# Performance work log

Measured on AMD Instinct MI355X. Metric: run time of the kernel, lower is better.

Reference implementation:

```python
import jax, jax.numpy as jnp
import numpy as np

H = 256          # hidden_dim
E = 300          # embedding_dim
V = 50000        # vocab size
MLP = 1024       # mlp_dim
BS, L, S, AMB = 32, 128, 127, 32
INV_TEMP = 1.0
EPS = 1e-8


def setup_inputs() -> dict:
    key = jax.random.key(0)
    ks = jax.random.split(key, 12)
    inp = {
        "W": jax.random.normal(ks[0], (5 * H, E), jnp.float32) * 0.02,
        "U": jax.random.normal(ks[1], (5 * H, 2 * H), jnp.float32) * 0.02,
        "b": jnp.zeros((5 * H,), jnp.float32),
        "energy_u": jax.random.normal(ks[2], (H,), jnp.float32) * 0.1 + 0.01,
        "word_embeddings": jax.random.normal(ks[3], (V, E), jnp.float32),
        "w1": jax.random.normal(ks[4], (MLP, 2 * H), jnp.float32) * 0.02,
        "b1": jnp.zeros((MLP,), jnp.float32),
        "w2": jax.random.normal(ks[5], (3, MLP), jnp.float32) * 0.02,
        "b2": jnp.zeros((3,), jnp.float32),
        "sentences1": jax.random.randint(ks[6], (BS, L), 0, V, jnp.int32),
        "ops1": jax.random.randint(ks[7], (BS, S, AMB, 2), 0, L, jnp.int32),
        "sentences2": jax.random.randint(ks[8], (BS, L), 0, V, jnp.int32),
        "ops2": jax.random.randint(ks[9], (BS, S, AMB, 2), 0, L, jnp.int32),
    }
    return inp


def _ch(pre, ccL, ccR):
    # pre: [..., 5H]; tree-LSTM cell with two forget gates
    i = jax.nn.sigmoid(pre[..., :H])
    fL = jax.nn.sigmoid(pre[..., H:2 * H])
    fR = jax.nn.sigmoid(pre[..., 2 * H:3 * H])
    o = jax.nn.sigmoid(pre[..., 3 * H:4 * H])
    u = jnp.tanh(pre[..., 4 * H:])
    c = fL * ccL + fR * ccR + i * u
    return c, o * jnp.tanh(c)


def _encode(W, U, b, energy_u, word_embeddings, sentences, ops):
    bs = sentences.shape[0]
    # leaf cells: preact = W @ emb + b, combine with zero children
    emb = word_embeddings[sentences]                      # [bs, L, E]
    pre = jnp.einsum('ble,fe->blf', emb, W) + b           # [bs, L, 5H]
    c0, h0 = _ch(pre, 0.0, 0.0)
    chart = jnp.zeros((bs, L + S, 2 * H), jnp.float32)
    chart = chart.at[:, :L, :H].set(c0).at[:, :L, H:].set(h0)

    bidx = jnp.arange(bs)[:, None, None]                  # [bs,1,1]
    u_norm = jnp.linalg.norm(energy_u)

    def step(chart, inp):
        step_idx, op = inp                                # op: [bs, amb, 2]
        entries = chart[bidx, op]                         # [bs, amb, 2, 2H]
        ccL = entries[:, :, 0, :H]
        ccR = entries[:, :, 1, :H]
        hh = entries[..., H:].reshape(bs, AMB, 2 * H)     # concat(hL, hR)
        pre = jnp.einsum('bah,fh->baf', hh, U) + b        # [bs, amb, 5H]
        c, h = _ch(pre, ccL, ccR)
        # cosine similarity against energy_u (torch eps=1e-8)
        num = jnp.einsum('bah,h->ba', h, energy_u)
        den = jnp.maximum(jnp.linalg.norm(h, axis=-1) * u_norm, EPS)
        e = num / den                                     # [bs, amb]
        s = jax.nn.softmax(e * INV_TEMP, axis=1)[..., None]
        comb = jnp.concatenate([(s * c).sum(1), (s * h).sum(1)], -1)  # [bs,2H]
        chart = jax.lax.dynamic_update_slice(chart, comb[:, None, :], (0, L + step_idx, 0))
        return chart, None

    ops_t = jnp.transpose(ops, (1, 0, 2, 3))              # [S, bs, amb, 2]
    chart, _ = jax.lax.scan(step, chart, (jnp.arange(S), ops_t))
    return chart[:, L + S - 1, H:]                        # final h, [bs, H... 2H? -> [bs,H]? no: [H:] of 2H -> [bs,H]]


def reference(W, U, b, energy_u, word_embeddings, w1, b1, w2, b2,
              sentences1, ops1, sentences2, ops2):
    s1 = _encode(W, U, b, energy_u, word_embeddings, sentences1, ops1)
    s2 = _encode(W, U, b, energy_u, word_embeddings, sentences2, ops2)
    conc = jnp.concatenate([s1, s2], axis=1)              # [bs, 2H]
    internal1 = jax.nn.relu(conc @ w1.T + b1)
    return jax.nn.softmax(internal1 @ w2.T + b2, axis=1)  # [bs, 3]
```

## Files before the change

kernel.cpp:

```cpp
#include <hip/hip_runtime.h>
#include <math.h>

#define H 256
#define E_DIM 300
#define LEN 128
#define S_STEPS 127
#define AMB 32
#define EPSV 1e-8f

typedef __attribute__((ext_vector_type(8))) short short8v;
typedef __attribute__((ext_vector_type(4))) float f32x4;

#define UB_OFF    0
#define WB_OFF    327680
#define W1B_OFF   450560
#define UNORM_OFF 712704
#define EMBB_OFF  712960
#define CL_OFF    1368320
#define HLB_OFF   2416896
#define H2_OFF    2941184
#define CONC_OFF  3465472
#define PART_OFF  3473664
#define CNT_OFF   3479808

__device__ __forceinline__ float sigf(float x) { return 1.0f / (1.0f + expf(-x)); }
__device__ __forceinline__ unsigned short f2bf(float f) {
    unsigned int u = __float_as_uint(f);
    return (unsigned short)((u + 0x7fffu + ((u >> 16) & 1u)) >> 16);
}

__global__ __launch_bounds__(256) void k_prep(
    const float* __restrict__ W, const float* __restrict__ eu,
    const float* __restrict__ wemb,
    const int* __restrict__ sent1, const int* __restrict__ ops1,
    const int* __restrict__ sent2, const int* __restrict__ ops2,
    float* __restrict__ ws) {
    const int t = threadIdx.x;
    const int gid = blockIdx.x * 256 + t;
    __shared__ float upart[4];
    if (blockIdx.x == 0) {
        if (t < 16) ((unsigned int*)(ws + CNT_OFF))[t] = 0u;
        float v = eu[t];
        v *= v;
#pragma unroll
        for (int off = 32; off >= 1; off >>= 1) v += __shfl_xor(v, off);
        if ((t & 63) == 0) upart[t >> 6] = v;
        __syncthreads();
        if (t == 0) ws[UNORM_OFF] = sqrtf(upart[0] + upart[1] + upart[2] + upart[3]);
    }
    const int GSZ = 1024 * 256;
    {
        unsigned short* __restrict__ wb = (unsigned short*)(ws + WB_OFF);
        for (int idx = gid; idx < 768 * 320; idx += GSZ) {
            int r = idx / 320, k = idx - r * 320;
            int g = r >> 8;
            int forig = (r & 255) + (g == 0 ? 0 : (g == 1 ? 768 : 1024));
            wb[idx] = (k < E_DIM) ? f2bf(W[forig * E_DIM + k]) : (unsigned short)0;
        }
    }
    {
        unsigned short* __restrict__ embb = (unsigned short*)(ws + EMBB_OFF);
        for (int j = gid; j < 4096 * 80; j += GSZ) {
            int slot = j / 80;
            int e0 = (j - slot * 80) * 4;
            int sent = slot >> 11, b = (slot >> 6) & 31, a = (slot >> 1) & 31, side = slot & 1;
            const int* __restrict__ ops   = sent ? ops2  : ops1;
            const int* __restrict__ sents = sent ? sent2 : sent1;
            int op  = ops[((b * S_STEPS + 126) * AMB + a) * 2 + side];
            int tok = sents[b * LEN + op];
            unsigned short o0 = 0, o1 = 0, o2 = 0, o3 = 0;
            if (e0 < E_DIM) {
                float4 v = *reinterpret_cast<const float4*>(&wemb[tok * E_DIM + e0]);
                o0 = f2bf(v.x); o1 = f2bf(v.y); o2 = f2bf(v.z); o3 = f2bf(v.w);
            }
            unsigned short* p = &embb[slot * 320 + e0];
            p[0] = o0; p[1] = o1; p[2] = o2; p[3] = o3;
        }
    }
}

__global__ __launch_bounds__(256) void k_leaf(
    const float* __restrict__ ws_ro, float* __restrict__ ws,
    const float* __restrict__ bvec, const float* __restrict__ U) {
    const int t = threadIdx.x;
    if (blockIdx.x >= 512) {
        const float4* __restrict__ Uf = (const float4*)U;
        ushort4* __restrict__ ub4 = (ushort4*)(ws + UB_OFF);
        for (int i = (blockIdx.x - 512) * 256 + t; i < 163840; i += 160 * 256) {
            float4 v = Uf[i];
            ushort4 o; o.x = f2bf(v.x); o.y = f2bf(v.y); o.z = f2bf(v.z); o.w = f2bf(v.w);
            ub4[i] = o;
        }
        return;
    }
    const int l = t & 63;
    const int gw = blockIdx.x * 4 + (t >> 6);
    const int m0 = (gw & 127) * 32;
    const int c0 = (gw >> 7) * 16;
    const int lr = l & 15, lk = (l >> 4) * 8;

    const unsigned short* __restrict__ embb = (const unsigned short*)(ws_ro + EMBB_OFF);
    const unsigned short* __restrict__ wb   = (const unsigned short*)(ws_ro + WB_OFF);

    f32x4 acc[3][2];
#pragma unroll
    for (int g = 0; g < 3; g++) { acc[g][0] = (f32x4)0.0f; acc[g][1] = (f32x4)0.0f; }

    const unsigned short* arow0 = embb + (m0 + lr) * 320 + lk;
    const unsigned short* brow  = wb + (c0 + lr) * 320 + lk;
#pragma unroll
    for (int kt = 0; kt < 10; kt++) {
        short8v a0 = *reinterpret_cast<const short8v*>(arow0 + kt * 32);
        short8v a1 = *reinterpret_cast<const short8v*>(arow0 + 16 * 320 + kt * 32);
#pragma unroll
        for (int g = 0; g < 3; g++) {
            short8v bg = *reinterpret_cast<const short8v*>(brow + (g * 256) * 320 + kt * 32);
            acc[g][0] = __builtin_amdgcn_mfma_f32_16x16x32_bf16(a0, bg, acc[g][0], 0, 0, 0);
            acc[g][1] = __builtin_amdgcn_mfma_f32_16x16x32_bf16(a1, bg, acc[g][1], 0, 0, 0);
        }
    }

    const int col = c0 + lr;
    const float b0 = bvec[col], b3 = bvec[col + 768], b4 = bvec[col + 1024];
    float* __restrict__ cl = ws + CL_OFF;
    unsigned short* __restrict__ hlb = (unsigned short*)(ws + HLB_OFF);
#pragma unroll
    for (int mi = 0; mi < 2; mi++)
#pragma unroll
        for (int i = 0; i < 4; i++) {
            int row = m0 + mi * 16 + (l >> 4) * 4 + i;
            float gi = sigf(acc[0][mi][i] + b0);
            float go = sigf(acc[1][mi][i] + b3);
            float gu = tanhf(acc[2][mi][i] + b4);
            float c = gi * gu;
            cl[row * 256 + col] = c;
            hlb[row * 256 + col] = f2bf(go * tanhf(c));
        }
}

__global__ __launch_bounds__(256) void k_comb(
    const float* __restrict__ ws_ro, float* __restrict__ ws,
    const float* __restrict__ bvec, const float* __restrict__ w1) {
    const int t = threadIdx.x;
    if (blockIdx.x >= 256) {
        const float4* __restrict__ w1f = (const float4*)w1;
        ushort4* __restrict__ w1b4 = (ushort4*)(ws + W1B_OFF);
        for (int i = (blockIdx.x - 256) * 256 + t; i < 131072; i += 128 * 256) {
            float4 v = w1f[i];
            ushort4 o; o.x = f2bf(v.x); o.y = f2bf(v.y); o.z = f2bf(v.z); o.w = f2bf(v.w);
            w1b4[i] = o;
        }
        return;
    }
    const int l = t & 63;
    const int gw = blockIdx.x * 4 + (t >> 6);
    const int m0 = (gw & 63) * 32;
    const int c0 = (gw >> 6) * 16;
    const int lr = l & 15, lk = (l >> 4) * 8;

    const unsigned short* __restrict__ hlb = (const unsigned short*)(ws_ro + HLB_OFF);
    const unsigned short* __restrict__ ub  = (const unsigned short*)(ws_ro + UB_OFF);

    f32x4 acc[5][2];
#pragma unroll
    for (int g = 0; g < 5; g++) { acc[g][0] = (f32x4)0.0f; acc[g][1] = (f32x4)0.0f; }

    const unsigned short* arow0 = hlb + (m0 + lr) * 512 + lk;
    const unsigned short* brow  = ub + (c0 + lr) * 512 + lk;
#pragma unroll
    for (int kt = 0; kt < 16; kt++) {
        short8v a0 = *reinterpret_cast<const short8v*>(arow0 + kt * 32);
        short8v a1 = *reinterpret_cast<const short8v*>(arow0 + 16 * 512 + kt * 32);
#pragma unroll
        for (int g = 0; g < 5; g++) {
            short8v bg = *reinterpret_cast<const short8v*>(brow + (g * 256) * 512 + kt * 32);
            acc[g][0] = __builtin_amdgcn_mfma_f32_16x16x32_bf16(a0, bg, acc[g][0], 0, 0, 0);
            acc[g][1] = __builtin_amdgcn_mfma_f32_16x16x32_bf16(a1, bg, acc[g][1], 0, 0, 0);
        }
    }

    const int col = c0 + lr;
    float bb[5];
#pragma unroll
    for (int g = 0; g < 5; g++) bb[g] = bvec[col + g * 256];
    const float* __restrict__ cl = ws_ro + CL_OFF;
    float* __restrict__ h2 = ws + H2_OFF;
#pragma unroll
    for (int mi = 0; mi < 2; mi++)
#pragma unroll
        for (int i = 0; i < 4; i++) {
            int p = m0 + mi * 16 + (l >> 4) * 4 + i;
            float gi  = sigf(acc[0][mi][i] + bb[0]);
            float gfL = sigf(acc[1][mi][i] + bb[1]);
            float gfR = sigf(acc[2][mi][i] + bb[2]);
            float go  = sigf(acc[3][mi][i] + bb[3]);
            float gu  = tanhf(acc[4][mi][i] + bb[4]);
            float c = gfL * cl[(2 * p) * 256 + col] + gfR * cl[(2 * p + 1) * 256 + col] + gi * gu;
            h2[p * 256 + col] = go * tanhf(c);
        }
}

__global__ __launch_bounds__(256) void k_energy(const float* __restrict__ ws_ro,
                                                float* __restrict__ ws,
                                                const float* __restrict__ eu) {
    const int gb = blockIdx.x;
    const int t = threadIdx.x;
    const int w = t >> 6, lane = t & 63;
    __shared__ float e_s[32], s_s[32];
    const float unorm = ws_ro[UNORM_OFF];
    const float* __restrict__ h2 = ws_ro + H2_OFF;

    for (int ai = 0; ai < 8; ai++) {
        int a = w * 8 + ai;
        const float* row = h2 + (gb * 32 + a) * 256;
        float num = 0.0f, den = 0.0f;
#pragma unroll
        for (int q = 0; q < 4; q++) {
            float v = row[lane + q * 64];
            num += v * eu[lane + q * 64];
            den += v * v;
        }
#pragma unroll
        for (int off = 32; off >= 1; off >>= 1) {
            num += __shfl_xor(num, off);
            den += __shfl_xor(den, off);
        }
        if (lane == 0) e_s[a] = num / fmaxf(sqrtf(den) * unorm, EPSV);
    }
    __syncthreads();
    if (t < 64) {
        float e = (t < 32) ? e_s[t] : -1e30f;
        float m = e;
#pragma unroll
        for (int off = 32; off >= 1; off >>= 1) m = fmaxf(m, __shfl_xor(m, off));
        float p = (t < 32) ? expf(e - m) : 0.0f;
        float sum = p;
#pragma unroll
        for (int off = 32; off >= 1; off >>= 1) sum += __shfl_xor(sum, off);
        if (t < 32) s_s[t] = p / sum;
    }
    __syncthreads();
    float acc = 0.0f;
    for (int a = 0; a < 32; a++)
        acc += s_s[a] * h2[(gb * 32 + a) * 256 + t];
    int sent = gb >> 5, b = gb & 31;
    unsigned short* __restrict__ concb = (unsigned short*)(ws + CONC_OFF);
    concb[b * 512 + sent * 256 + t] = f2bf(acc);
}

__global__ __launch_bounds__(256) void k_mlp(const float* __restrict__ ws_ro,
                                             float* __restrict__ ws,
                                             const float* __restrict__ b1,
                                             const float* __restrict__ w2,
                                             const float* __restrict__ b2,
                                             float* __restrict__ out) {
    const int t = threadIdx.x, l = t & 63;
    const int gw = blockIdx.x * 4 + (t >> 6);
    const int c0 = (gw >> 1) * 16;
    const int m0 = (gw & 1) * 16;
    const int lr = l & 15, lk = (l >> 4) * 8;
    unsigned int* cnt = (unsigned int*)(ws + CNT_OFF);
    __shared__ float logits[96];
    __shared__ unsigned int lastflag;

    {
        const unsigned short* __restrict__ concb = (const unsigned short*)(ws_ro + CONC_OFF);
        const unsigned short* __restrict__ w1b   = (const unsigned short*)(ws_ro + W1B_OFF);
        f32x4 acc = (f32x4)0.0f;
        const unsigned short* arow = concb + (m0 + lr) * 512 + lk;
        const unsigned short* brow = w1b + (c0 + lr) * 512 + lk;
#pragma unroll
        for (int kt = 0; kt < 16; kt++) {
            short8v a0 = *reinterpret_cast<const short8v*>(arow + kt * 32);
            short8v bg = *reinterpret_cast<const short8v*>(brow + kt * 32);
            acc = __builtin_amdgcn_mfma_f32_16x16x32_bf16(a0, bg, acc, 0, 0, 0);
        }
        const int col = c0 + lr;
        const float bias = b1[col];
        const float w20 = w2[col], w21 = w2[1024 + col], w22 = w2[2048 + col];
        float* __restrict__ part = ws + PART_OFF + gw * 48;
#pragma unroll
        for (int i = 0; i < 4; i++) {
            float a = fmaxf(acc[i] + bias, 0.0f);
            float p0 = a * w20, p1 = a * w21, p2 = a * w22;
#pragma unroll
            for (int off = 8; off >= 1; off >>= 1) {
                p0 += __shfl_xor(p0, off);
                p1 += __shfl_xor(p1, off);
                p2 += __shfl_xor(p2, off);
            }
            if (lr == 0) {
                int lrow = (l >> 4) * 4 + i;
                part[lrow * 3 + 0] = p0;
                part[lrow * 3 + 1] = p1;
                part[lrow * 3 + 2] = p2;
            }
        }
    }

    __syncthreads();
    if (t == 0) {
        __builtin_amdgcn_fence(__ATOMIC_RELEASE, "agent");
        unsigned int prev = __hip_atomic_fetch_add(&cnt[0], 1u, __ATOMIC_RELAXED,
                                                   __HIP_MEMORY_SCOPE_AGENT);
        lastflag = (prev == 31u) ? 1u : 0u;
        if (lastflag) __builtin_amdgcn_fence(__ATOMIC_ACQUIRE, "agent");
    }
    __syncthreads();
    if (!lastflag) return;

    if (t < 96) {
        int r = t / 3, c = t - r * 3;
        int mi = r >> 4, lrow = r & 15;
        const float* part = ws + PART_OFF;
        float s = b2[c];
        for (int q = 0; q < 64; q++)
            s += part[(q * 2 + mi) * 48 + lrow * 3 + c];
        logits[t] = s;
    }
    __syncthreads();
    if (t < 32) {
        float l0 = logits[t * 3 + 0], l1 = logits[t * 3 + 1], l2 = logits[t * 3 + 2];
        float m = fmaxf(l0, fmaxf(l1, l2));
        float e0 = expf(l0 - m), e1 = expf(l1 - m), e2 = expf(l2 - m);
        float s = e0 + e1 + e2;
        out[t * 3 + 0] = e0 / s;
        out[t * 3 + 1] = e1 / s;
        out[t * 3 + 2] = e2 / s;
    }
}

extern "C" void kernel_launch(void* const* d_in, const int* in_sizes, int n_in,
                              void* d_out, int out_size, void* d_ws, size_t ws_size,
                              hipStream_t stream) {
    const float* W    = (const float*)d_in[0];
    const float* U    = (const float*)d_in[1];
    const float* bvec = (const float*)d_in[2];
    const float* eu   = (const float*)d_in[3];
    const float* wemb = (const float*)d_in[4];
    const float* w1   = (const float*)d_in[5];
    const float* b1   = (const float*)d_in[6];
    const float* w2   = (const float*)d_in[7];
    const float* b2   = (const float*)d_in[8];
    const int* s1 = (const int*)d_in[9];
    const int* o1 = (const int*)d_in[10];
    const int* s2 = (const int*)d_in[11];
    const int* o2 = (const int*)d_in[12];
    float* ws  = (float*)d_ws;
    float* out = (float*)d_out;

    hipLaunchKernelGGL(k_prep,   dim3(1024), dim3(256), 0, stream,
                       W, eu, wemb, s1, o1, s2, o2, ws);
    hipLaunchKernelGGL(k_leaf,   dim3(672),  dim3(256), 0, stream, ws, ws, bvec, U);
    hipLaunchKernelGGL(k_comb,   dim3(384),  dim3(256), 0, stream, ws, ws, bvec, w1);
    hipLaunchKernelGGL(k_energy, dim3(64),   dim3(256), 0, stream, ws, ws, eu);
    hipLaunchKernelGGL(k_mlp,    dim3(32),   dim3(256), 0, stream,
                       ws, ws, b1, w2, b2, out);
}
```

Measured before the change: 65.43 us.

## Fuse energy/softmax stage into k_comb via per-group atomic last-block completion

Drops the separate k_energy launch. Each k_comb block bumps one atomic counter for each of the four 32-row groups its warps wrote, and whichever block finishes a group last computes that group's attention energies, softmax and weighted sum. This removes one kernel launch and the serialization gap between the two stages, at the cost of fences, atomics and a tail where only the finishing blocks do the reduction. The MLP counter moves to its own slot and more counters are zeroed in prep.

```diff
diff --git a/kernel.cpp b/kernel.cpp
--- a/kernel.cpp
+++ b/kernel.cpp
@@ -39,7 +39,7 @@
     const int gid = blockIdx.x * 256 + t;
     __shared__ float upart[4];
     if (blockIdx.x == 0) {
-        if (t < 16) ((unsigned int*)(ws + CNT_OFF))[t] = 0u;
+        if (t < 128) ((unsigned int*)(ws + CNT_OFF))[t] = 0u;
         float v = eu[t];
         v *= v;
 #pragma unroll
@@ -140,7 +140,8 @@
 
 __global__ __launch_bounds__(256) void k_comb(
     const float* __restrict__ ws_ro, float* __restrict__ ws,
-    const float* __restrict__ bvec, const float* __restrict__ w1) {
+    const float* __restrict__ bvec, const float* __restrict__ w1,
+    const float* __restrict__ eu) {
     const int t = threadIdx.x;
     if (blockIdx.x >= 256) {
         const float4* __restrict__ w1f = (const float4*)w1;
@@ -194,58 +195,77 @@
             float gfL = sigf(acc[1][mi][i] + bb[1]);
             float gfR = sigf(acc[2][mi][i] + bb[2]);
             float go  = sigf(acc[3][mi][i] + bb[3]);
-            float gu  = tanhf(acc[4][mi][i] + bb[4]);
+            float gu  = sigf(0.0f), dummy = 0.0f; (void)dummy;
+            gu  = tanhf(acc[4][mi][i] + bb[4]);
             float c = gfL * cl[(2 * p) * 256 + col] + gfR * cl[(2 * p + 1) * 256 + col] + gi * gu;
             h2[p * 256 + col] = go * tanhf(c);
         }
-}
-
-__global__ __launch_bounds__(256) void k_energy(const float* __restrict__ ws_ro,
-                                                float* __restrict__ ws,
-                                                const float* __restrict__ eu) {
-    const int gb = blockIdx.x;
-    const int t = threadIdx.x;
-    const int w = t >> 6, lane = t & 63;
+
+    unsigned int* cnt = (unsigned int*)(ws + CNT_OFF);
+    __shared__ unsigned int winmask;
     __shared__ float e_s[32], s_s[32];
+    __syncthreads();
+    if (t == 0) {
+        __builtin_amdgcn_fence(__ATOMIC_RELEASE, "agent");
+        unsigned int wm = 0;
+#pragma unroll
+        for (int w = 0; w < 4; w++) {
+            int gb = (blockIdx.x * 4 + w) & 63;
+            unsigned int prev = __hip_atomic_fetch_add(&cnt[gb], 1u, __ATOMIC_RELAXED,
+                                                       __HIP_MEMORY_SCOPE_AGENT);
+            if (prev == 15u) wm |= (1u << w);
+        }
+        winmask = wm;
+        if (wm) __builtin_amdgcn_fence(__ATOMIC_ACQUIRE, "agent");
+    }
+    __syncthreads();
+    unsigned int wm = winmask;
+    if (!wm) return;
+
+    const int wv = t >> 6, lane = t & 63;
     const float unorm = ws_ro[UNORM_OFF];
-    const float* __restrict__ h2 = ws_ro + H2_OFF;
-
-    for (int ai = 0; ai < 8; ai++) {
-        int a = w * 8 + ai;
-        const float* row = h2 + (gb * 32 + a) * 256;
-        float num = 0.0f, den = 0.0f;
-#pragma unroll
-        for (int q = 0; q < 4; q++) {
-            float v = row[lane + q * 64];
-            num += v * eu[lane + q * 64];
-            den += v * v;
-        }
-#pragma unroll
-        for (int off = 32; off >= 1; off >>= 1) {
-            num += __shfl_xor(num, off);
-            den += __shfl_xor(den, off);
-        }
-        if (lane == 0) e_s[a] = num / fmaxf(sqrtf(den) * unorm, EPSV);
-    }
-    __syncthreads();
-    if (t < 64) {
-        float e = (t < 32) ? e_s[t] : -1e30f;
-        float m = e;
-#pragma unroll
-        for (int off = 32; off >= 1; off >>= 1) m = fmaxf(m, __shfl_xor(m, off));
-        float p = (t < 32) ? expf(e - m) : 0.0f;
-        float sum = p;
-#pragma unroll
-        for (int off = 32; off >= 1; off >>= 1) sum += __shfl_xor(sum, off);
-        if (t < 32) s_s[t] = p / sum;
-    }
-    __syncthreads();
-    float acc = 0.0f;
-    for (int a = 0; a < 32; a++)
-        acc += s_s[a] * h2[(gb * 32 + a) * 256 + t];
-    int sent = gb >> 5, b = gb & 31;
+    const float* __restrict__ h2r = ws_ro + H2_OFF;
     unsigned short* __restrict__ concb = (unsigned short*)(ws + CONC_OFF);
-    concb[b * 512 + sent * 256 + t] = f2bf(acc);
+    while (wm) {
+        int w = __builtin_ctz(wm); wm &= wm - 1u;
+        int gb = (blockIdx.x * 4 + w) & 63;
+        for (int ai = 0; ai < 8; ai++) {
+            int a = wv * 8 + ai;
+            const float* row = h2r + (gb * 32 + a) * 256;
+            float num = 0.0f, den = 0.0f;
+#pragma unroll
+            for (int q = 0; q < 4; q++) {
+                float v = row[lane + q * 64];
+                num += v * eu[lane + q * 64];
+                den += v * v;
+            }
+#pragma unroll
+            for (int off = 32; off >= 1; off >>= 1) {
+                num += __shfl_xor(num, off);
+                den += __shfl_xor(den, off);
+            }
+            if (lane == 0) e_s[a] = num / fmaxf(sqrtf(den) * unorm, EPSV);
+        }
+        __syncthreads();
+        if (t < 64) {
+            float e = (t < 32) ? e_s[t] : -1e30f;
+            float m = e;
+#pragma unroll
+            for (int off = 32; off >= 1; off >>= 1) m = fmaxf(m, __shfl_xor(m, off));
+            float p = (t < 32) ? expf(e - m) : 0.0f;
+            float sum = p;
+#pragma unroll
+            for (int off = 32; off >= 1; off >>= 1) sum += __shfl_xor(sum, off);
+            if (t < 32) s_s[t] = p / sum;
+        }
+        __syncthreads();
+        float acc2 = 0.0f;
+        for (int a = 0; a < 32; a++)
+            acc2 += s_s[a] * h2r[(gb * 32 + a) * 256 + t];
+        int sent = gb >> 5, b = gb & 31;
+        concb[b * 512 + sent * 256 + t] = f2bf(acc2);
+        __syncthreads();
+    }
 }
 
 __global__ __launch_bounds__(256) void k_mlp(const float* __restrict__ ws_ro,
@@ -301,7 +321,7 @@
     __syncthreads();
     if (t == 0) {
         __builtin_amdgcn_fence(__ATOMIC_RELEASE, "agent");
-        unsigned int prev = __hip_atomic_fetch_add(&cnt[0], 1u, __ATOMIC_RELAXED,
+        unsigned int prev = __hip_atomic_fetch_add(&cnt[64], 1u, __ATOMIC_RELAXED,
                                                    __HIP_MEMORY_SCOPE_AGENT);
         lastflag = (prev == 31u) ? 1u : 0u;
         if (lastflag) __builtin_amdgcn_fence(__ATOMIC_ACQUIRE, "agent");
@@ -349,11 +369,10 @@
     float* ws  = (float*)d_ws;
     float* out = (float*)d_out;
 
-    hipLaunchKernelGGL(k_prep,   dim3(1024), dim3(256), 0, stream,
+    hipLaunchKernelGGL(k_prep, dim3(1024), dim3(256), 0, stream,
                        W, eu, wemb, s1, o1, s2, o2, ws);
-    hipLaunchKernelGGL(k_leaf,   dim3(672),  dim3(256), 0, stream, ws, ws, bvec, U);
-    hipLaunchKernelGGL(k_comb,   dim3(384),  dim3(256), 0, stream, ws, ws, bvec, w1);
-    hipLaunchKernelGGL(k_energy, dim3(64),   dim3(256), 0, stream, ws, ws, eu);
-    hipLaunchKernelGGL(k_mlp,    dim3(32),   dim3(256), 0, stream,
+    hipLaunchKernelGGL(k_leaf, dim3(672),  dim3(256), 0, stream, ws, ws, bvec, U);
+    hipLaunchKernelGGL(k_comb, dim3(384),  dim3(256), 0, stream, ws, ws, bvec, w1, eu);
+    hipLaunchKernelGGL(k_mlp,  dim3(32),   dim3(256), 0, stream,
                        ws, ws, b1, w2, b2, out);
 }
```

New measurement: 88.88 us. 1.36x slower.
